# Optimization experiments

Hardware: AMD Instinct MI355X
Metric: run time of the kernel (lower is better)

The kernel has to match this reference:

```python
import jax, jax.numpy as jnp
import numpy as np

IN_SIZE = 3072
HIDDEN = 32
OUT_SIZE = 10
N = 32768


def setup_inputs() -> dict:
    key = jax.random.key(0)
    kx, k1, kb1, k2, kb2 = jax.random.split(key, 5)
    x = jax.random.normal(kx, (N, IN_SIZE), dtype=jnp.float32)
    # torch.nn.Linear default init scale ~ 1/sqrt(fan_in); use scaled normals
    W1 = jax.random.normal(k1, (HIDDEN, IN_SIZE), dtype=jnp.float32) / np.sqrt(IN_SIZE)
    b1 = jax.random.normal(kb1, (HIDDEN,), dtype=jnp.float32) / np.sqrt(IN_SIZE)
    W2 = jax.random.normal(k2, (OUT_SIZE, HIDDEN), dtype=jnp.float32) / np.sqrt(HIDDEN)
    b2 = jax.random.normal(kb2, (OUT_SIZE,), dtype=jnp.float32) / np.sqrt(HIDDEN)
    return {"x": x, "W1": W1, "b1": b1, "W2": W2, "b2": b2}


def reference(x, W1, b1, W2, b2):
    # Batched equivalent of the per-sample loop:
    # y[i] = sigmoid(lin2(relu(lin1(x[i]))))
    h = jax.nn.relu(jnp.einsum('ni,hi->nh', x, W1) + b1)   # (N, 32)
    out = jnp.einsum('nh,oh->no', h, W2) + b2              # (N, out_size)
    return jax.nn.sigmoid(out)
```

## Files before the change

### kernel.cpp

```cpp
#include <hip/hip_runtime.h>
#include <hip/hip_bf16.h>


typedef float  f32x4  __attribute__((ext_vector_type(4)));
typedef short  short8 __attribute__((ext_vector_type(8)));

#define IN_SIZE 3072
#define KSTEPS  96
#define HIDDEN  32
#define OUTS    10

__device__ __forceinline__ unsigned short f2bf(float f) {
    return __builtin_bit_cast(unsigned short, __float2bfloat16(f));
}

__device__ __forceinline__ short8 cvt8(f32x4 a, f32x4 b) {
    short8 r;
    r[0] = (short)f2bf(a[0]); r[1] = (short)f2bf(a[1]);
    r[2] = (short)f2bf(a[2]); r[3] = (short)f2bf(a[3]);
    r[4] = (short)f2bf(b[0]); r[5] = (short)f2bf(b[1]);
    r[6] = (short)f2bf(b[2]); r[7] = (short)f2bf(b[3]);
    return r;
}

__global__ void prep_w1(const float* __restrict__ W1,
                        unsigned short* __restrict__ w1s) {
    int t  = blockIdx.x * 256 + threadIdx.x;
    int l  = t & 63;
    int nt = (t >> 6) & 1;
    int s  = t >> 7;
    int h  = (l & 15) + nt * 16;
    int k  = s * 32 + ((l >> 4) * 8);
    const float* src = W1 + (size_t)h * IN_SIZE + k;
    f32x4 f0 = *(const f32x4*)src;
    f32x4 f1 = *(const f32x4*)(src + 4);
    ((short8*)w1s)[t] = cvt8(f0, f1);
}

template <bool USE_WS>
__global__ __launch_bounds__(256, 2)
void mlp_fused(const float* __restrict__ x,
               const float* __restrict__ W1,
               const float* __restrict__ b1,
               const float* __restrict__ W2,
               const float* __restrict__ b2,
               const unsigned short* __restrict__ w1s,
               float* __restrict__ out) {
    __shared__ __align__(16) float hbuf[4][16][36];

    const int tid = threadIdx.x;
    const int l   = tid & 63;
    const int w   = tid >> 6;
    const int lr  = l & 15;
    const int kg  = l >> 4;
    const int rowbase = blockIdx.x * 64 + w * 16;

    const float* xp = x + (size_t)(rowbase + lr) * IN_SIZE + kg * 8;

    f32x4 acc0 = {0.f, 0.f, 0.f, 0.f};
    f32x4 acc1 = {0.f, 0.f, 0.f, 0.f};

    if constexpr (USE_WS) {
        const short8* wp = (const short8*)w1s + l;
        f32x4 a0 = *(const f32x4*)(xp);
        f32x4 a1 = *(const f32x4*)(xp + 4);
        short8 bf0 = wp[0];
        short8 bf1 = wp[64];
        #pragma unroll 4
        for (int s = 0; s < KSTEPS; ++s) {
            const int sn = (s + 1 < KSTEPS) ? s + 1 : KSTEPS - 1;
            f32x4 na0 = *(const f32x4*)(xp + sn * 32);
            f32x4 na1 = *(const f32x4*)(xp + sn * 32 + 4);
            short8 nb0 = wp[sn * 128];
            short8 nb1 = wp[sn * 128 + 64];
            short8 af = cvt8(a0, a1);
            acc0 = __builtin_amdgcn_mfma_f32_16x16x32_bf16(af, bf0, acc0, 0, 0, 0);
            acc1 = __builtin_amdgcn_mfma_f32_16x16x32_bf16(af, bf1, acc1, 0, 0, 0);
            a0 = na0; a1 = na1; bf0 = nb0; bf1 = nb1;
        }
    } else {
        const float* w0p = W1 + (size_t)lr * IN_SIZE + kg * 8;
        const float* w1p = W1 + (size_t)(lr + 16) * IN_SIZE + kg * 8;
        f32x4 a0 = *(const f32x4*)(xp);
        f32x4 a1 = *(const f32x4*)(xp + 4);
        f32x4 c0 = *(const f32x4*)(w0p);
        f32x4 c1 = *(const f32x4*)(w0p + 4);
        f32x4 d0 = *(const f32x4*)(w1p);
        f32x4 d1 = *(const f32x4*)(w1p + 4);
        #pragma unroll 4
        for (int s = 0; s < KSTEPS; ++s) {
            const int sn = (s + 1 < KSTEPS) ? s + 1 : KSTEPS - 1;
            f32x4 na0 = *(const f32x4*)(xp + sn * 32);
            f32x4 na1 = *(const f32x4*)(xp + sn * 32 + 4);
            f32x4 nc0 = *(const f32x4*)(w0p + sn * 32);
            f32x4 nc1 = *(const f32x4*)(w0p + sn * 32 + 4);
            f32x4 nd0 = *(const f32x4*)(w1p + sn * 32);
            f32x4 nd1 = *(const f32x4*)(w1p + sn * 32 + 4);
            short8 af = cvt8(a0, a1);
            short8 bf0 = cvt8(c0, c1);
            short8 bf1 = cvt8(d0, d1);
            acc0 = __builtin_amdgcn_mfma_f32_16x16x32_bf16(af, bf0, acc0, 0, 0, 0);
            acc1 = __builtin_amdgcn_mfma_f32_16x16x32_bf16(af, bf1, acc1, 0, 0, 0);
            a0 = na0; a1 = na1; c0 = nc0; c1 = nc1; d0 = nd0; d1 = nd1;
        }
    }

    const float bv0 = b1[lr];
    const float bv1 = b1[lr + 16];
    #pragma unroll
    for (int i = 0; i < 4; ++i) {
        float v0 = acc0[i] + bv0; v0 = v0 > 0.f ? v0 : 0.f;
        float v1 = acc1[i] + bv1; v1 = v1 > 0.f ? v1 : 0.f;
        hbuf[w][kg * 4 + i][lr]      = v0;
        hbuf[w][kg * 4 + i][lr + 16] = v1;
    }
    __syncthreads();

    if (l < 32) {
        const int half = l >> 4;
        const int row  = l & 15;
        f32x4 hv[8];
        const f32x4* hp = (const f32x4*)&hbuf[w][row][0];
        #pragma unroll
        for (int q = 0; q < 8; ++q) hv[q] = hp[q];

        const int rg = rowbase + row;
        float* op = out + (size_t)rg * OUTS + half * 5;
        #pragma unroll
        for (int oo = 0; oo < 5; ++oo) {
            const int o = half * 5 + oo;
            const f32x4* w2p = (const f32x4*)(W2 + o * HIDDEN);
            f32x4 s4 = {0.f, 0.f, 0.f, 0.f};
            #pragma unroll
            for (int q = 0; q < 8; ++q) s4 += hv[q] * w2p[q];
            float v = b2[o] + s4[0] + s4[1] + s4[2] + s4[3];
            op[oo] = 1.0f / (1.0f + __expf(-v));
        }
    }
}

extern "C" void kernel_launch(void* const* d_in, const int* in_sizes, int n_in,
                              void* d_out, int out_size, void* d_ws, size_t ws_size,
                              hipStream_t stream) {
    (void)n_in; (void)out_size;
    const float* x  = (const float*)d_in[0];
    const float* W1 = (const float*)d_in[1];
    const float* b1 = (const float*)d_in[2];
    const float* W2 = (const float*)d_in[3];
    const float* b2 = (const float*)d_in[4];
    float* out = (float*)d_out;

    const int N = in_sizes[0] / IN_SIZE;
    const int nblocks = N / 64;

    const size_t ws_needed = (size_t)KSTEPS * 128 * 16;
    if (ws_size >= ws_needed) {
        unsigned short* w1s = (unsigned short*)d_ws;
        prep_w1<<<dim3(48), dim3(256), 0, stream>>>(W1, w1s);
        mlp_fused<true><<<dim3(nblocks), dim3(256), 0, stream>>>(
            x, W1, b1, W2, b2, w1s, out);
    } else {
        mlp_fused<false><<<dim3(nblocks), dim3(256), 0, stream>>>(
            x, W1, b1, W2, b2, nullptr, out);
    }
}
```

Baseline: 93.02 us.

## Split K across wave pairs and reduce partial sums in shared memory

Each block now covers 32 rows, and two waves split the 3072-long reduction per 16-row group, so the grid doubles and each wave has half the serial K loop. Partial accumulators are combined in LDS before bias, ReLU and the second layer. The main loop is rewritten with a two-deep manual register prefetch, and launch bounds now ask for 4 blocks per CU. The intent is more memory parallelism for this bandwidth-bound x stream, at the cost of extra LDS traffic and higher register pressure under the tighter occupancy bound.

```diff
diff --git a/kernel.cpp b/kernel.cpp
--- a/kernel.cpp
+++ b/kernel.cpp
@@ -6,9 +6,10 @@
 typedef short  short8 __attribute__((ext_vector_type(8)));
 
 #define IN_SIZE 3072
-#define KSTEPS  96
 #define HIDDEN  32
 #define OUTS    10
+#define KSPLIT  2
+#define KH      (IN_SIZE / 32 / KSPLIT)
 
 __device__ __forceinline__ unsigned short f2bf(float f) {
     return __builtin_bit_cast(unsigned short, __float2bfloat16(f));
@@ -38,7 +39,7 @@
 }
 
 template <bool USE_WS>
-__global__ __launch_bounds__(256, 2)
+__global__ __launch_bounds__(256, 4)
 void mlp_fused(const float* __restrict__ x,
                const float* __restrict__ W1,
                const float* __restrict__ b1,
@@ -46,41 +47,60 @@
                const float* __restrict__ b2,
                const unsigned short* __restrict__ w1s,
                float* __restrict__ out) {
-    __shared__ __align__(16) float hbuf[4][16][36];
+    __shared__ __align__(16) float hbuf[2][2][16][36];
 
     const int tid = threadIdx.x;
     const int l   = tid & 63;
     const int w   = tid >> 6;
+    const int rg  = w >> 1;
+    const int kh  = w & 1;
     const int lr  = l & 15;
     const int kg  = l >> 4;
-    const int rowbase = blockIdx.x * 64 + w * 16;
+    const int rowbase = blockIdx.x * 32 + rg * 16;
 
-    const float* xp = x + (size_t)(rowbase + lr) * IN_SIZE + kg * 8;
+    const float* xp = x + (size_t)(rowbase + lr) * IN_SIZE + kh * (KH * 32) + kg * 8;
 
     f32x4 acc0 = {0.f, 0.f, 0.f, 0.f};
     f32x4 acc1 = {0.f, 0.f, 0.f, 0.f};
 
     if constexpr (USE_WS) {
-        const short8* wp = (const short8*)w1s + l;
-        f32x4 a0 = *(const f32x4*)(xp);
-        f32x4 a1 = *(const f32x4*)(xp + 4);
-        short8 bf0 = wp[0];
-        short8 bf1 = wp[64];
-        #pragma unroll 4
-        for (int s = 0; s < KSTEPS; ++s) {
-            const int sn = (s + 1 < KSTEPS) ? s + 1 : KSTEPS - 1;
-            f32x4 na0 = *(const f32x4*)(xp + sn * 32);
-            f32x4 na1 = *(const f32x4*)(xp + sn * 32 + 4);
-            short8 nb0 = wp[sn * 128];
-            short8 nb1 = wp[sn * 128 + 64];
-            short8 af = cvt8(a0, a1);
-            acc0 = __builtin_amdgcn_mfma_f32_16x16x32_bf16(af, bf0, acc0, 0, 0, 0);
-            acc1 = __builtin_amdgcn_mfma_f32_16x16x32_bf16(af, bf1, acc1, 0, 0, 0);
-            a0 = na0; a1 = na1; bf0 = nb0; bf1 = nb1;
+        const short8* wp = (const short8*)w1s + (size_t)kh * KH * 128 + l;
+        f32x4 pa0 = *(const f32x4*)(xp);
+        f32x4 pa1 = *(const f32x4*)(xp + 4);
+        short8 pb0 = wp[0];
+        short8 pb1 = wp[64];
+        f32x4 qa0 = *(const f32x4*)(xp + 32);
+        f32x4 qa1 = *(const f32x4*)(xp + 36);
+        short8 qb0 = wp[128];
+        short8 qb1 = wp[192];
+        int s = 0;
+        for (; s + 2 < KH; s += 2) {
+            short8 af = cvt8(pa0, pa1);
+            acc0 = __builtin_amdgcn_mfma_f32_16x16x32_bf16(af, pb0, acc0, 0, 0, 0);
+            acc1 = __builtin_amdgcn_mfma_f32_16x16x32_bf16(af, pb1, acc1, 0, 0, 0);
+            pa0 = *(const f32x4*)(xp + (s + 2) * 32);
+            pa1 = *(const f32x4*)(xp + (s + 2) * 32 + 4);
+            pb0 = wp[(s + 2) * 128];
+            pb1 = wp[(s + 2) * 128 + 64];
+            short8 ag = cvt8(qa0, qa1);
+            acc0 = __builtin_amdgcn_mfma_f32_16x16x32_bf16(ag, qb0, acc0, 0, 0, 0);
+            acc1 = __builtin_amdgcn_mfma_f32_16x16x32_bf16(ag, qb1, acc1, 0, 0, 0);
+            if (s + 3 < KH) {
+                qa0 = *(const f32x4*)(xp + (s + 3) * 32);
+                qa1 = *(const f32x4*)(xp + (s + 3) * 32 + 4);
+                qb0 = wp[(s + 3) * 128];
+                qb1 = wp[(s + 3) * 128 + 64];
+            }
         }
+        short8 af = cvt8(pa0, pa1);
+        acc0 = __builtin_amdgcn_mfma_f32_16x16x32_bf16(af, pb0, acc0, 0, 0, 0);
+        acc1 = __builtin_amdgcn_mfma_f32_16x16x32_bf16(af, pb1, acc1, 0, 0, 0);
+        short8 ag = cvt8(qa0, qa1);
+        acc0 = __builtin_amdgcn_mfma_f32_16x16x32_bf16(ag, qb0, acc0, 0, 0, 0);
+        acc1 = __builtin_amdgcn_mfma_f32_16x16x32_bf16(ag, qb1, acc1, 0, 0, 0);
     } else {
-        const float* w0p = W1 + (size_t)lr * IN_SIZE + kg * 8;
-        const float* w1p = W1 + (size_t)(lr + 16) * IN_SIZE + kg * 8;
+        const float* w0p = W1 + (size_t)lr * IN_SIZE + kh * (KH * 32) + kg * 8;
+        const float* w1p = W1 + (size_t)(lr + 16) * IN_SIZE + kh * (KH * 32) + kg * 8;
         f32x4 a0 = *(const f32x4*)(xp);
         f32x4 a1 = *(const f32x4*)(xp + 4);
         f32x4 c0 = *(const f32x4*)(w0p);
@@ -88,15 +108,15 @@
         f32x4 d0 = *(const f32x4*)(w1p);
         f32x4 d1 = *(const f32x4*)(w1p + 4);
         #pragma unroll 4
-        for (int s = 0; s < KSTEPS; ++s) {
-            const int sn = (s + 1 < KSTEPS) ? s + 1 : KSTEPS - 1;
+        for (int s = 0; s < KH; ++s) {
+            const int sn = (s + 1 < KH) ? s + 1 : KH - 1;
             f32x4 na0 = *(const f32x4*)(xp + sn * 32);
             f32x4 na1 = *(const f32x4*)(xp + sn * 32 + 4);
             f32x4 nc0 = *(const f32x4*)(w0p + sn * 32);
             f32x4 nc1 = *(const f32x4*)(w0p + sn * 32 + 4);
             f32x4 nd0 = *(const f32x4*)(w1p + sn * 32);
             f32x4 nd1 = *(const f32x4*)(w1p + sn * 32 + 4);
-            short8 af = cvt8(a0, a1);
+            short8 af  = cvt8(a0, a1);
             short8 bf0 = cvt8(c0, c1);
             short8 bf1 = cvt8(d0, d1);
             acc0 = __builtin_amdgcn_mfma_f32_16x16x32_bf16(af, bf0, acc0, 0, 0, 0);
@@ -105,27 +125,30 @@
         }
     }
 
-    const float bv0 = b1[lr];
-    const float bv1 = b1[lr + 16];
     #pragma unroll
     for (int i = 0; i < 4; ++i) {
-        float v0 = acc0[i] + bv0; v0 = v0 > 0.f ? v0 : 0.f;
-        float v1 = acc1[i] + bv1; v1 = v1 > 0.f ? v1 : 0.f;
-        hbuf[w][kg * 4 + i][lr]      = v0;
-        hbuf[w][kg * 4 + i][lr + 16] = v1;
+        hbuf[rg][kh][kg * 4 + i][lr]      = acc0[i];
+        hbuf[rg][kh][kg * 4 + i][lr + 16] = acc1[i];
     }
     __syncthreads();
 
-    if (l < 32) {
+    if (kh == 0 && l < 32) {
         const int half = l >> 4;
         const int row  = l & 15;
+        const f32x4* hp0 = (const f32x4*)&hbuf[rg][0][row][0];
+        const f32x4* hp1 = (const f32x4*)&hbuf[rg][1][row][0];
+        const f32x4* bb  = (const f32x4*)b1;
         f32x4 hv[8];
-        const f32x4* hp = (const f32x4*)&hbuf[w][row][0];
         #pragma unroll
-        for (int q = 0; q < 8; ++q) hv[q] = hp[q];
+        for (int q = 0; q < 8; ++q) {
+            f32x4 v = hp0[q] + hp1[q] + bb[q];
+            #pragma unroll
+            for (int j = 0; j < 4; ++j) v[j] = fmaxf(v[j], 0.f);
+            hv[q] = v;
+        }
 
-        const int rg = rowbase + row;
-        float* op = out + (size_t)rg * OUTS + half * 5;
+        const int rgrow = rowbase + row;
+        float* op = out + (size_t)rgrow * OUTS + half * 5;
         #pragma unroll
         for (int oo = 0; oo < 5; ++oo) {
             const int o = half * 5 + oo;
@@ -151,9 +174,9 @@
     float* out = (float*)d_out;
 
     const int N = in_sizes[0] / IN_SIZE;
-    const int nblocks = N / 64;
+    const int nblocks = N / 32;
 
-    const size_t ws_needed = (size_t)KSTEPS * 128 * 16;
+    const size_t ws_needed = (size_t)(IN_SIZE / 32) * 128 * 16;
     if (ws_size >= ws_needed) {
         unsigned short* w1s = (unsigned short*)d_ws;
         prep_w1<<<dim3(48), dim3(256), 0, stream>>>(W1, w1s);
```

After: 89.52 us. -3.8%, faster.

## Stage x and W1 tiles through LDS with async global_load_lds double buffering

Applied to the files above, without the earlier changes.

Replaces the per-lane register prefetch loop with a double-buffered LDS pipeline. Each stage uses global_load_lds to bring 128 K-columns of the 64 x-rows and the matching bf16 W1 slices into shared memory, then computes from LDS while the next stage loads. The goal is to keep more bytes in flight and get contiguous row loads for x. It adds 80KB of LDS per block, which may limit occupancy to one block per CU, and adds two barriers per stage.

```diff
diff --git a/kernel.cpp b/kernel.cpp
--- a/kernel.cpp
+++ b/kernel.cpp
@@ -6,9 +6,12 @@
 typedef short  short8 __attribute__((ext_vector_type(8)));
 
 #define IN_SIZE 3072
-#define KSTEPS  96
+#define ROWB    (IN_SIZE * 4)
 #define HIDDEN  32
 #define OUTS    10
+#define NSTAGE  24
+#define ABUF_SZ 32768
+#define BBUF_SZ 8192
 
 __device__ __forceinline__ unsigned short f2bf(float f) {
     return __builtin_bit_cast(unsigned short, __float2bfloat16(f));
@@ -37,16 +40,21 @@
     ((short8*)w1s)[t] = cvt8(f0, f1);
 }
 
-template <bool USE_WS>
+typedef __attribute__((address_space(3))) void        lds_void;
+typedef const __attribute__((address_space(1))) void  gm_void;
+
+__device__ __forceinline__ void gload16(const void* g, void* l) {
+    __builtin_amdgcn_global_load_lds((gm_void*)g, (lds_void*)l, 16, 0, 0);
+}
+
 __global__ __launch_bounds__(256, 2)
-void mlp_fused(const float* __restrict__ x,
-               const float* __restrict__ W1,
-               const float* __restrict__ b1,
-               const float* __restrict__ W2,
-               const float* __restrict__ b2,
-               const unsigned short* __restrict__ w1s,
-               float* __restrict__ out) {
-    __shared__ __align__(16) float hbuf[4][16][36];
+void mlp_staged(const float* __restrict__ x,
+                const float* __restrict__ b1,
+                const float* __restrict__ W2,
+                const float* __restrict__ b2,
+                const unsigned short* __restrict__ w1s,
+                float* __restrict__ out) {
+    __shared__ __align__(16) unsigned char pool[2 * ABUF_SZ + 2 * BBUF_SZ];
 
     const int tid = threadIdx.x;
     const int l   = tid & 63;
@@ -55,56 +63,134 @@
     const int kg  = l >> 4;
     const int rowbase = blockIdx.x * 64 + w * 16;
 
-    const float* xp = x + (size_t)(rowbase + lr) * IN_SIZE + kg * 8;
+    char* ldsA = (char*)pool;
+    char* ldsB = (char*)pool + 2 * ABUF_SZ;
+
+    const char* xw   = (const char*)x + (size_t)rowbase * ROWB;
+    const char* wsrc = (const char*)w1s;
+    const int   rpair = l >> 5;
+    const int   pos   = (l & 31) * 16;
 
     f32x4 acc0 = {0.f, 0.f, 0.f, 0.f};
     f32x4 acc1 = {0.f, 0.f, 0.f, 0.f};
 
-    if constexpr (USE_WS) {
-        const short8* wp = (const short8*)w1s + l;
-        f32x4 a0 = *(const f32x4*)(xp);
-        f32x4 a1 = *(const f32x4*)(xp + 4);
-        short8 bf0 = wp[0];
-        short8 bf1 = wp[64];
-        #pragma unroll 4
-        for (int s = 0; s < KSTEPS; ++s) {
-            const int sn = (s + 1 < KSTEPS) ? s + 1 : KSTEPS - 1;
-            f32x4 na0 = *(const f32x4*)(xp + sn * 32);
-            f32x4 na1 = *(const f32x4*)(xp + sn * 32 + 4);
-            short8 nb0 = wp[sn * 128];
-            short8 nb1 = wp[sn * 128 + 64];
+    auto issue = [&](int t) {
+        const int buf = t & 1;
+        char* da = ldsA + buf * ABUF_SZ + w * 8192;
+        const char* xs = xw + (size_t)t * 512 + (size_t)rpair * ROWB + pos;
+        #pragma unroll
+        for (int j = 0; j < 8; ++j)
+            gload16(xs + (size_t)(2 * j) * ROWB, da + j * 1024);
+        char* db = ldsB + buf * BBUF_SZ;
+        #pragma unroll
+        for (int c = 0; c < 2; ++c) {
+            const int p = 2 * w + c;
+            const char* src = wsrc +
+                ((size_t)((t * 4 + (p >> 1)) * 128 + (p & 1) * 64 + l)) * 16;
+            gload16(src, db + p * 1024);
+        }
+    };
+
+    auto compute = [&](int t) {
+        const int buf = t & 1;
+        const char* A = ldsA + buf * ABUF_SZ + w * 8192 + lr * 512 + kg * 32;
+        const char* B = ldsB + buf * BBUF_SZ + l * 16;
+        #pragma unroll
+        for (int s = 0; s < 4; ++s) {
+            f32x4 a0  = *(const f32x4*)(A + s * 128);
+            f32x4 a1  = *(const f32x4*)(A + s * 128 + 16);
+            short8 bf0 = *(const short8*)(B + (2 * s) * 1024);
+            short8 bf1 = *(const short8*)(B + (2 * s + 1) * 1024);
             short8 af = cvt8(a0, a1);
             acc0 = __builtin_amdgcn_mfma_f32_16x16x32_bf16(af, bf0, acc0, 0, 0, 0);
             acc1 = __builtin_amdgcn_mfma_f32_16x16x32_bf16(af, bf1, acc1, 0, 0, 0);
-            a0 = na0; a1 = na1; bf0 = nb0; bf1 = nb1;
-        }
-    } else {
-        const float* w0p = W1 + (size_t)lr * IN_SIZE + kg * 8;
-        const float* w1p = W1 + (size_t)(lr + 16) * IN_SIZE + kg * 8;
-        f32x4 a0 = *(const f32x4*)(xp);
-        f32x4 a1 = *(const f32x4*)(xp + 4);
-        f32x4 c0 = *(const f32x4*)(w0p);
-        f32x4 c1 = *(const f32x4*)(w0p + 4);
-        f32x4 d0 = *(const f32x4*)(w1p);
-        f32x4 d1 = *(const f32x4*)(w1p + 4);
-        #pragma unroll 4
-        for (int s = 0; s < KSTEPS; ++s) {
-            const int sn = (s + 1 < KSTEPS) ? s + 1 : KSTEPS - 1;
-            f32x4 na0 = *(const f32x4*)(xp + sn * 32);
-            f32x4 na1 = *(const f32x4*)(xp + sn * 32 + 4);
-            f32x4 nc0 = *(const f32x4*)(w0p + sn * 32);
-            f32x4 nc1 = *(const f32x4*)(w0p + sn * 32 + 4);
-            f32x4 nd0 = *(const f32x4*)(w1p + sn * 32);
-            f32x4 nd1 = *(const f32x4*)(w1p + sn * 32 + 4);
-            short8 af = cvt8(a0, a1);
-            short8 bf0 = cvt8(c0, c1);
-            short8 bf1 = cvt8(d0, d1);
-            acc0 = __builtin_amdgcn_mfma_f32_16x16x32_bf16(af, bf0, acc0, 0, 0, 0);
-            acc1 = __builtin_amdgcn_mfma_f32_16x16x32_bf16(af, bf1, acc1, 0, 0, 0);
-            a0 = na0; a1 = na1; c0 = nc0; c1 = nc1; d0 = nd0; d1 = nd1;
-        }
-    }
-
+        }
+    };
+
+    issue(0);
+    #pragma unroll 1
+    for (int t = 0; t < NSTAGE; ++t) {
+        if (t + 1 < NSTAGE) {
+            issue(t + 1);
+            asm volatile("s_waitcnt vmcnt(10)" ::: "memory");
+        } else {
+            asm volatile("s_waitcnt vmcnt(0)" ::: "memory");
+        }
+        __builtin_amdgcn_s_barrier();
+        compute(t);
+        asm volatile("" ::: "memory");
+        __builtin_amdgcn_s_barrier();
+    }
+
+    float* hb = (float*)pool + w * (16 * 36);
+    const float bv0 = b1[lr];
+    const float bv1 = b1[lr + 16];
+    #pragma unroll
+    for (int i = 0; i < 4; ++i) {
+        float v0 = acc0[i] + bv0; v0 = v0 > 0.f ? v0 : 0.f;
+        float v1 = acc1[i] + bv1; v1 = v1 > 0.f ? v1 : 0.f;
+        hb[(kg * 4 + i) * 36 + lr]      = v0;
+        hb[(kg * 4 + i) * 36 + lr + 16] = v1;
+    }
+    __syncthreads();
+
+    if (l < 32) {
+        const int half = l >> 4;
+        const int row  = l & 15;
+        f32x4 hv[8];
+        const f32x4* hp = (const f32x4*)&hb[row * 36];
+        #pragma unroll
+        for (int q = 0; q < 8; ++q) hv[q] = hp[q];
+
+        float* op = out + (size_t)(rowbase + row) * OUTS + half * 5;
+        #pragma unroll
+        for (int oo = 0; oo < 5; ++oo) {
+            const int o = half * 5 + oo;
+            const f32x4* w2p = (const f32x4*)(W2 + o * HIDDEN);
+            f32x4 s4 = {0.f, 0.f, 0.f, 0.f};
+            #pragma unroll
+            for (int q = 0; q < 8; ++q) s4 += hv[q] * w2p[q];
+            float v = b2[o] + s4[0] + s4[1] + s4[2] + s4[3];
+            op[oo] = 1.0f / (1.0f + __expf(-v));
+        }
+    }
+}
+
+__global__ __launch_bounds__(256, 2)
+void mlp_fallback(const float* __restrict__ x,
+                  const float* __restrict__ W1,
+                  const float* __restrict__ b1,
+                  const float* __restrict__ W2,
+                  const float* __restrict__ b2,
+                  float* __restrict__ out) {
+    __shared__ __align__(16) float hbuf[4][16][36];
+    const int tid = threadIdx.x;
+    const int l   = tid & 63;
+    const int w   = tid >> 6;
+    const int lr  = l & 15;
+    const int kg  = l >> 4;
+    const int rowbase = blockIdx.x * 64 + w * 16;
+
+    const float* xp  = x + (size_t)(rowbase + lr) * IN_SIZE + kg * 8;
+    const float* w0p = W1 + (size_t)lr * IN_SIZE + kg * 8;
+    const float* w1p = W1 + (size_t)(lr + 16) * IN_SIZE + kg * 8;
+
+    f32x4 acc0 = {0.f, 0.f, 0.f, 0.f};
+    f32x4 acc1 = {0.f, 0.f, 0.f, 0.f};
+    #pragma unroll 4
+    for (int s = 0; s < IN_SIZE / 32; ++s) {
+        f32x4 a0 = *(const f32x4*)(xp + s * 32);
+        f32x4 a1 = *(const f32x4*)(xp + s * 32 + 4);
+        f32x4 c0 = *(const f32x4*)(w0p + s * 32);
+        f32x4 c1 = *(const f32x4*)(w0p + s * 32 + 4);
+        f32x4 d0 = *(const f32x4*)(w1p + s * 32);
+        f32x4 d1 = *(const f32x4*)(w1p + s * 32 + 4);
+        short8 af  = cvt8(a0, a1);
+        short8 bf0 = cvt8(c0, c1);
+        short8 bf1 = cvt8(d0, d1);
+        acc0 = __builtin_amdgcn_mfma_f32_16x16x32_bf16(af, bf0, acc0, 0, 0, 0);
+        acc1 = __builtin_amdgcn_mfma_f32_16x16x32_bf16(af, bf1, acc1, 0, 0, 0);
+    }
     const float bv0 = b1[lr];
     const float bv1 = b1[lr + 16];
     #pragma unroll
@@ -115,7 +201,6 @@
         hbuf[w][kg * 4 + i][lr + 16] = v1;
     }
     __syncthreads();
-
     if (l < 32) {
         const int half = l >> 4;
         const int row  = l & 15;
@@ -123,9 +208,7 @@
         const f32x4* hp = (const f32x4*)&hbuf[w][row][0];
         #pragma unroll
         for (int q = 0; q < 8; ++q) hv[q] = hp[q];
-
-        const int rg = rowbase + row;
-        float* op = out + (size_t)rg * OUTS + half * 5;
+        float* op = out + (size_t)(rowbase + row) * OUTS + half * 5;
         #pragma unroll
         for (int oo = 0; oo < 5; ++oo) {
             const int o = half * 5 + oo;
@@ -153,14 +236,14 @@
     const int N = in_sizes[0] / IN_SIZE;
     const int nblocks = N / 64;
 
-    const size_t ws_needed = (size_t)KSTEPS * 128 * 16;
+    const size_t ws_needed = (size_t)(IN_SIZE / 32) * 128 * 16;
     if (ws_size >= ws_needed) {
         unsigned short* w1s = (unsigned short*)d_ws;
         prep_w1<<<dim3(48), dim3(256), 0, stream>>>(W1, w1s);
-        mlp_fused<true><<<dim3(nblocks), dim3(256), 0, stream>>>(
-            x, W1, b1, W2, b2, w1s, out);
+        mlp_staged<<<dim3(nblocks), dim3(256), 0, stream>>>(
+            x, b1, W2, b2, w1s, out);
     } else {
-        mlp_fused<false><<<dim3(nblocks), dim3(256), 0, stream>>>(
-            x, W1, b1, W2, b2, nullptr, out);
-    }
-}
+        mlp_fallback<<<dim3(nblocks), dim3(256), 0, stream>>>(
+            x, W1, b1, W2, b2, out);
+    }
+}
```

Result: no change. 92.65 us (-0.4%).
